# Kernel optimization log

Measured on AMD Instinct MI355X. Metric: run time of the kernel, lower is better.

Reference implementation:

```python
import jax, jax.numpy as jnp
import numpy as np

K = 64  # nodes kept per graph (SortPooling k)

def setup_inputs() -> dict:
    key = jax.random.key(0)
    N, D = 131072, 256  # 256 graphs x 512 nodes
    feat = jax.random.normal(key, (N, D), dtype=jnp.float32)
    return {"feat": feat, "num_graphs": 256}

def reference(feat, num_graphs):
    # feat: (N, D) node features; batched graph of `num_graphs` equal-sized graphs
    N, D = feat.shape
    n = N // num_graphs  # nodes per graph
    # 1) sort each node's feature vector ascending along feature dim (tf.sort(feat, -1))
    feat_s = jnp.sort(feat, axis=-1)
    # 2) segmented top-k: rank nodes within each graph by the LAST feature value
    #    (sortby=-1), descending, and keep k nodes (DGL topk_nodes semantics)
    fb = feat_s.reshape(num_graphs, n, D)  # (B, n, D)
    scores = fb[:, :, -1]                  # (B, n) = max of each sorted row
    _, idx = jax.lax.top_k(scores, K)      # descending order, (B, k)
    topk = jnp.take_along_axis(fb, idx[:, :, None], axis=1)  # (B, k, D)
    # 3) flatten to (B, k*D)
    return topk.reshape(num_graphs, K * D)
```

## Files before the change

### kernel.cpp

```cpp
#include <hip/hip_runtime.h>
#include <hip/hip_bf16.h>

#define NROWS   131072
#define D       256
#define NGRAPH  256
#define NPG     512
#define KSEL    64

__global__ __launch_bounds__(256) void row_max_kernel(const float* __restrict__ feat,
                                                      float* __restrict__ scores) {
    const int gtid = blockIdx.x * blockDim.x + threadIdx.x;
    const int row  = gtid >> 6;
    const int lane = threadIdx.x & 63;
    if (row >= NROWS) return;

    const float4 v = reinterpret_cast<const float4*>(feat + (size_t)row * D)[lane];
    float m = fmaxf(fmaxf(v.x, v.y), fmaxf(v.z, v.w));
#pragma unroll
    for (int off = 32; off > 0; off >>= 1)
        m = fmaxf(m, __shfl_xor(m, off));
    if (lane == 0) scores[row] = m;
}

__global__ __launch_bounds__(512) void topk_kernel(const float* __restrict__ scores,
                                                   int* __restrict__ idx_out) {
    __shared__ float s[NPG];
    __shared__ int   id[NPG];
    const int g = blockIdx.x;
    const int t = threadIdx.x;

    s[t]  = scores[g * NPG + t];
    id[t] = t;
    __syncthreads();

    for (int k = 2; k <= NPG; k <<= 1) {
        for (int j = k >> 1; j > 0; j >>= 1) {
            const int ixj = t ^ j;
            if (ixj > t) {
                const float s1 = s[t], s2 = s[ixj];
                const int   i1 = id[t], i2 = id[ixj];
                const bool before = (s1 > s2) || (s1 == s2 && i1 < i2);
                const bool up     = ((t & k) == 0);
                if (up ? !before : before) {
                    s[t] = s2; s[ixj] = s1;
                    id[t] = i2; id[ixj] = i1;
                }
            }
            __syncthreads();
        }
    }

    if (t < KSEL) idx_out[g * KSEL + t] = g * NPG + id[t];
}

__global__ __launch_bounds__(256) void sort_row_kernel(const float* __restrict__ feat,
                                                       const int* __restrict__ idx,
                                                       float* __restrict__ out) {
    __shared__ float s[D];
    const int b = blockIdx.x;
    const int t = threadIdx.x;
    const int row = idx[b];

    s[t] = feat[(size_t)row * D + t];
    __syncthreads();

    for (int k = 2; k <= D; k <<= 1) {
        for (int j = k >> 1; j > 0; j >>= 1) {
            const int ixj = t ^ j;
            if (ixj > t) {
                const float a = s[t], c = s[ixj];
                const bool up = ((t & k) == 0);
                if (up ? (a > c) : (a < c)) { s[t] = c; s[ixj] = a; }
            }
            __syncthreads();
        }
    }

    out[(size_t)b * D + t] = s[t];
}

extern "C" void kernel_launch(void* const* d_in, const int* in_sizes, int n_in,
                              void* d_out, int out_size, void* d_ws, size_t ws_size,
                              hipStream_t stream) {
    const float* feat = (const float*)d_in[0];
    float* out = (float*)d_out;

    float* scores = (float*)d_ws;
    int*   idx    = (int*)((char*)d_ws + (size_t)NROWS * sizeof(float));

    row_max_kernel<<<NROWS / 4, 256, 0, stream>>>(feat, scores);

    topk_kernel<<<NGRAPH, NPG, 0, stream>>>(scores, idx);

    sort_row_kernel<<<NGRAPH * KSEL, D, 0, stream>>>(feat, idx, out);
}
```

Baseline: 253.2 us.

## Sort rows in registers per wavefront and batch four rows per wave in row-max

The per-row bitonic sort moves from a block-wide shared-memory sort with a barrier after every step to a single wavefront holding four elements per lane. Cross-lane steps use shuffles and cross-register steps use in-register min/max, so the 36 block barriers and the shared-memory traffic go away, and each block now handles four rows. Row-max also processes four rows per wave, which cuts the launch size and the number of shuffle reductions per row. The register sort's direction logic is hand-derived, so a mistake there would produce wrong order.

```diff
diff --git a/kernel.cpp b/kernel.cpp
--- a/kernel.cpp
+++ b/kernel.cpp
@@ -9,17 +9,29 @@
 
 __global__ __launch_bounds__(256) void row_max_kernel(const float* __restrict__ feat,
                                                       float* __restrict__ scores) {
-    const int gtid = blockIdx.x * blockDim.x + threadIdx.x;
-    const int row  = gtid >> 6;
+    const int wave = (blockIdx.x * 256 + threadIdx.x) >> 6;
     const int lane = threadIdx.x & 63;
-    if (row >= NROWS) return;
+    const int row0 = wave * 4;
 
-    const float4 v = reinterpret_cast<const float4*>(feat + (size_t)row * D)[lane];
-    float m = fmaxf(fmaxf(v.x, v.y), fmaxf(v.z, v.w));
+    const float4* p = reinterpret_cast<const float4*>(feat) + (size_t)row0 * 64 + lane;
+    const float4 a = p[0], b = p[64], c = p[128], d = p[192];
+
+    float m0 = fmaxf(fmaxf(a.x, a.y), fmaxf(a.z, a.w));
+    float m1 = fmaxf(fmaxf(b.x, b.y), fmaxf(b.z, b.w));
+    float m2 = fmaxf(fmaxf(c.x, c.y), fmaxf(c.z, c.w));
+    float m3 = fmaxf(fmaxf(d.x, d.y), fmaxf(d.z, d.w));
+
 #pragma unroll
-    for (int off = 32; off > 0; off >>= 1)
-        m = fmaxf(m, __shfl_xor(m, off));
-    if (lane == 0) scores[row] = m;
+    for (int off = 32; off > 0; off >>= 1) {
+        m0 = fmaxf(m0, __shfl_xor(m0, off));
+        m1 = fmaxf(m1, __shfl_xor(m1, off));
+        m2 = fmaxf(m2, __shfl_xor(m2, off));
+        m3 = fmaxf(m3, __shfl_xor(m3, off));
+    }
+    if (lane < 4) {
+        const float m = (lane == 0) ? m0 : (lane == 1) ? m1 : (lane == 2) ? m2 : m3;
+        scores[row0 + lane] = m;
+    }
 }
 
 __global__ __launch_bounds__(512) void topk_kernel(const float* __restrict__ scores,
@@ -56,27 +68,54 @@
 __global__ __launch_bounds__(256) void sort_row_kernel(const float* __restrict__ feat,
                                                        const int* __restrict__ idx,
                                                        float* __restrict__ out) {
-    __shared__ float s[D];
-    const int b = blockIdx.x;
-    const int t = threadIdx.x;
-    const int row = idx[b];
+    const int wv   = threadIdx.x >> 6;
+    const int lane = threadIdx.x & 63;
+    const int b    = blockIdx.x * 4 + wv;
+    const int row  = idx[b];
 
-    s[t] = feat[(size_t)row * D + t];
-    __syncthreads();
+    const float* src = feat + (size_t)row * D;
+    float v[4];
+#pragma unroll
+    for (int r = 0; r < 4; ++r) v[r] = src[r * 64 + lane];
 
-    for (int k = 2; k <= D; k <<= 1) {
+#pragma unroll
+    for (int k = 2; k <= 256; k <<= 1) {
+#pragma unroll
         for (int j = k >> 1; j > 0; j >>= 1) {
-            const int ixj = t ^ j;
-            if (ixj > t) {
-                const float a = s[t], c = s[ixj];
-                const bool up = ((t & k) == 0);
-                if (up ? (a > c) : (a < c)) { s[t] = c; s[ixj] = a; }
+            if (j >= 64) {
+                const int rb = j >> 6;
+#pragma unroll
+                for (int r = 0; r < 4; ++r) {
+                    if ((r & rb) == 0) {
+                        const int rp = r | rb;
+                        const bool up = (k == 256) ? true : ((r & 2) == 0);
+                        const float mn = fminf(v[r], v[rp]);
+                        const float mx = fmaxf(v[r], v[rp]);
+                        v[r]  = up ? mn : mx;
+                        v[rp] = up ? mx : mn;
+                    }
+                }
+            } else {
+#pragma unroll
+                for (int r = 0; r < 4; ++r) {
+                    const float o = __shfl_xor(v[r], j);
+                    bool up;
+                    if      (k <= 32)  up = ((lane & k) == 0);
+                    else if (k == 64)  up = ((r & 1) == 0);
+                    else if (k == 128) up = ((r & 2) == 0);
+                    else               up = true;
+                    const bool lower = ((lane & j) == 0);
+                    const float mn = fminf(v[r], o);
+                    const float mx = fmaxf(v[r], o);
+                    v[r] = (up == lower) ? mn : mx;
+                }
             }
-            __syncthreads();
         }
     }
 
-    out[(size_t)b * D + t] = s[t];
+    float* dst = out + (size_t)b * D;
+#pragma unroll
+    for (int r = 0; r < 4; ++r) dst[r * 64 + lane] = v[r];
 }
 
 extern "C" void kernel_launch(void* const* d_in, const int* in_sizes, int n_in,
@@ -88,9 +127,9 @@
     float* scores = (float*)d_ws;
     int*   idx    = (int*)((char*)d_ws + (size_t)NROWS * sizeof(float));
 
-    row_max_kernel<<<NROWS / 4, 256, 0, stream>>>(feat, scores);
+    row_max_kernel<<<NROWS / 16, 256, 0, stream>>>(feat, scores);
 
     topk_kernel<<<NGRAPH, NPG, 0, stream>>>(scores, idx);
 
-    sort_row_kernel<<<NGRAPH * KSEL, D, 0, stream>>>(feat, idx, out);
+    sort_row_kernel<<<NGRAPH * KSEL / 4, 256, 0, stream>>>(feat, idx, out);
 }
```

New measurement: 225.3 us. -11.0%, faster.
